# Performance work log

Measured on AMD Instinct MI355X. Metric: run time of the kernel, lower is better.

Reference implementation:

```python
import jax, jax.numpy as jnp
import numpy as np

EPS = 1e-5

def _fftfreq(n, d):
    k = jnp.concatenate([jnp.arange(0, (n + 1) // 2), jnp.arange(-(n // 2), 0)]).astype(jnp.float32)
    return k / (n * d)

def _inorm(x):
    # InstanceNorm2d, no affine, biased variance, eps=1e-5; x: (B,C,H,W)
    m = jnp.mean(x, axis=(-2, -1), keepdims=True)
    v = jnp.var(x, axis=(-2, -1), keepdims=True)
    return (x - m) / jnp.sqrt(v + EPS)

def _spectral_conv(x, t_grid, x_grid, p1, p2, res):
    # x: (B, C, Sx, Sy) real; p1:(in,out,m1) p2:(in,out,m2) res:(in,out,m1,m2) complex64
    B, C, Sx, Sy = x.shape
    dty = x_grid[0, 1] - x_grid[0, 0]
    dtx = t_grid[0, 1] - t_grid[0, 0]
    alpha = jnp.fft.fft2(x, axes=(-2, -1))  # (B,in,Sx,Sy) complex
    om1 = (_fftfreq(Sx, dty) * (2 * jnp.pi) * 1j).astype(jnp.complex64)  # (Sx,)
    om2 = (_fftfreq(Sy, dtx) * (2 * jnp.pi) * 1j).astype(jnp.complex64)  # (Sy,)
    d1 = om1[:, None, None, None] - p1  # (Sx,in,out,m1)
    d2 = om2[:, None, None, None] - p2  # (Sy,in,out,m2)
    denom = jnp.einsum('pbix,qbik->pqbixk', d1, d2)  # (Sx,Sy,in,out,m1,m2)
    Hw = res[None, None] / denom  # pole-residue rational kernel
    r1 = jnp.einsum('biox,oxikpq->bkox', alpha, Hw)  # (B,out,Sx,Sy)
    r2 = jnp.einsum('biox,oxikpq->bkpq', alpha, Hw)  # (B,out,m1,m2)
    x1 = jnp.real(jnp.fft.ifft2(r1, s=(Sx, Sy), axes=(-2, -1)))
    ty_c = x_grid.reshape(1, -1).astype(jnp.complex64)  # (1,Sx)
    tx_c = t_grid.reshape(1, -1).astype(jnp.complex64)  # (1,Sy)
    e1 = jnp.exp(jnp.einsum('bip,kz->bipz', p1, ty_c))  # (in,out,m1,Sx)
    e2 = jnp.exp(jnp.einsum('biq,kx->biqx', p2, tx_c))  # (in,out,m2,Sy)
    term3 = jnp.einsum('bipz,biqx->bipqzx', e1, e2)     # (in,out,m1,m2,Sx,Sy)
    x2 = jnp.real(jnp.einsum('kbpq,bipqzx->kizx', r2, term3)) / (Sx * Sy)
    return x1 + x2

def reference(x, fc0_w, fc0_b, p1r, p1i, p2r, p2i, resr, resi,
              w0_w, w0_b, fc1_w, fc1_b, fc2_w, fc2_b, t_grid, x_grid):
    B, Sx, Sy, _ = x.shape
    gx = jnp.broadcast_to(jnp.linspace(0.0, 1.0, Sx, dtype=jnp.float32)[None, :, None, None], (B, Sx, Sy, 1))
    gy = jnp.broadcast_to(jnp.linspace(0.0, 1.0, Sy, dtype=jnp.float32)[None, None, :, None], (B, Sx, Sy, 1))
    h = jnp.concatenate([x, gx, gy], axis=-1)           # (B,Sx,Sy,3)
    h = h @ fc0_w.T + fc0_b                              # (B,Sx,Sy,16)
    h = h.transpose(0, 3, 1, 2)                          # (B,16,Sx,Sy)
    p1 = (p1r + 1j * p1i).astype(jnp.complex64)
    p2 = (p2r + 1j * p2i).astype(jnp.complex64)
    res = (resr + 1j * resi).astype(jnp.complex64)
    x1 = _inorm(_spectral_conv(_inorm(h), t_grid, x_grid, p1, p2, res))
    x2 = jnp.einsum('bihw,oi->bohw', h, w0_w) + w0_b[None, :, None, None]  # 1x1 conv
    h = x1 + x2
    h = h.transpose(0, 2, 3, 1)                          # (B,Sx,Sy,16)
    h = jnp.sin(h @ fc1_w.T + fc1_b)                     # (B,Sx,Sy,128)
    h = h @ fc2_w.T + fc2_b                              # (B,Sx,Sy,1)
    return h

def setup_inputs() -> dict:
    key = jax.random.key(0)
    ks = jax.random.split(key, 16)
    W, M1, M2, B, S = 16, 4, 5, 4, 64
    scale = 1.0 / (W * W)
    inp = {
        'x': jax.random.normal(ks[0], (B, S, S, 1), jnp.float32),
        'fc0_w': jax.random.normal(ks[1], (W, 3), jnp.float32) * 0.3,
        'fc0_b': jax.random.normal(ks[2], (W,), jnp.float32) * 0.1,
        'p1r': jax.random.uniform(ks[3], (W, W, M1), jnp.float32) * scale,
        'p1i': jax.random.uniform(ks[4], (W, W, M1), jnp.float32) * scale,
        'p2r': jax.random.uniform(ks[5], (W, W, M2), jnp.float32) * scale,
        'p2i': jax.random.uniform(ks[6], (W, W, M2), jnp.float32) * scale,
        'resr': jax.random.uniform(ks[7], (W, W, M1, M2), jnp.float32) * scale,
        'resi': jax.random.uniform(ks[8], (W, W, M1, M2), jnp.float32) * scale,
        'w0_w': jax.random.normal(ks[9], (W, W), jnp.float32) * 0.25,
        'w0_b': jax.random.normal(ks[10], (W,), jnp.float32) * 0.1,
        'fc1_w': jax.random.normal(ks[11], (128, W), jnp.float32) * 0.25,
        'fc1_b': jax.random.normal(ks[12], (128,), jnp.float32) * 0.1,
        'fc2_w': jax.random.normal(ks[13], (1, 128), jnp.float32) * 0.1,
        'fc2_b': jax.random.normal(ks[14], (1,), jnp.float32) * 0.1,
        't_grid': jnp.linspace(0.0, 1.0, S, dtype=jnp.float32).reshape(1, S),
        'x_grid': jnp.linspace(0.0, 1.0, S, dtype=jnp.float32).reshape(1, S),
    }
    return inp
```

## Files before the change

### kernel.cpp

```cpp
#include <hip/hip_runtime.h>

typedef float2 cplx;

constexpr float TWO_PI = 6.28318530717958647692f;

__device__ inline void cmac(float& ax, float& ay, cplx a, cplx b) {
    ax += a.x * b.x - a.y * b.y;
    ay += a.x * b.y + a.y * b.x;
}

__global__ __launch_bounds__(256) void k_pre(
    const float* __restrict__ x, const float* __restrict__ fc0_w,
    const float* __restrict__ fc0_b,
    const float* __restrict__ p1r, const float* __restrict__ p1i,
    const float* __restrict__ p2r, const float* __restrict__ p2i,
    const float* __restrict__ resr, const float* __restrict__ resi,
    const float* __restrict__ t_grid, const float* __restrict__ x_grid,
    cplx* __restrict__ A, cplx* __restrict__ Bq, cplx* __restrict__ Cq,
    cplx* __restrict__ e1, cplx* __restrict__ e2,
    float* __restrict__ h, float* __restrict__ accH2)
{
    int idx = blockIdx.x * 256 + threadIdx.x;
    float dty = x_grid[1] - x_grid[0];
    float dtx = t_grid[1] - t_grid[0];
    const int NA = 65536, NBQ = 81920, NCQ = 81920, NE1 = 65536, NE2 = 81920;
    if (idx < NA) {
        int p = idx & 3, k = (idx >> 2) & 15, i = (idx >> 6) & 15, o = idx >> 10;
        int kf = (o < 32) ? o : o - 64;
        float om = TWO_PI * (float)kf / (64.f * dty);
        float dr = -p1r[(i * 16 + k) * 4 + p], di = om - p1i[(i * 16 + k) * 4 + p];
        float inv = 1.f / (dr * dr + di * di);
        A[idx] = make_float2(dr * inv, -di * inv);
        return;
    }
    idx -= NA;
    if (idx < NBQ) {
        int q = idx % 5, k = (idx / 5) & 15, i = (idx / 80) & 15, xx = idx / 1280;
        int kf = (xx < 32) ? xx : xx - 64;
        float om = TWO_PI * (float)kf / (64.f * dtx);
        float dr = -p2r[(i * 16 + k) * 5 + q], di = om - p2i[(i * 16 + k) * 5 + q];
        float inv = 1.f / (dr * dr + di * di);
        Bq[idx] = make_float2(dr * inv, -di * inv);
        return;
    }
    idx -= NBQ;
    if (idx < NCQ) {
        int q = idx % 5, k = (idx / 5) & 15, i = (idx / 80) & 15, o = idx / 1280;
        int kf = (o < 32) ? o : o - 64;
        float om = TWO_PI * (float)kf / (64.f * dty);
        float cx = 0.f, cy = 0.f;
        for (int p = 0; p < 4; ++p) {
            float dr = -p1r[(i * 16 + k) * 4 + p], di = om - p1i[(i * 16 + k) * 4 + p];
            float inv = 1.f / (dr * dr + di * di);
            float axr = dr * inv, axi = -di * inv;
            float rr = resr[((i * 16 + k) * 4 + p) * 5 + q];
            float ri = resi[((i * 16 + k) * 4 + p) * 5 + q];
            cx += rr * axr - ri * axi;
            cy += rr * axi + ri * axr;
        }
        Cq[idx] = make_float2(cx, cy);
        return;
    }
    idx -= NCQ;
    if (idx < NE1) {
        int z = idx & 63, w = idx >> 6;
        float t = x_grid[z];
        float m = expf(p1r[w] * t);
        float sn, cs; sincosf(p1i[w] * t, &sn, &cs);
        e1[idx] = make_float2(m * cs, m * sn);
        return;
    }
    idx -= NE1;
    if (idx < NE2) {
        int xx = idx & 63, w = idx >> 6;
        float t = t_grid[xx];
        float m = expf(p2r[w] * t);
        float sn, cs; sincosf(p2i[w] * t, &sn, &cs);
        e2[idx] = make_float2(m * cs, m * sn);
        return;
    }
    idx -= NE2;
    {
        int bc = idx >> 12, pix = idx & 4095;
        int b = bc >> 4, c = bc & 15;
        int z = pix >> 6, xx = pix & 63;
        const float inv63 = 1.f / 63.f;
        float v = fc0_w[c * 3] * x[b * 4096 + pix]
                + fc0_w[c * 3 + 1] * (z * inv63)
                + fc0_w[c * 3 + 2] * (xx * inv63) + fc0_b[c];
        h[idx] = v;
        float s = v, s2 = v * v;
        for (int m = 32; m; m >>= 1) {
            s  += __shfl_xor(s,  m, 64);
            s2 += __shfl_xor(s2, m, 64);
        }
        if ((threadIdx.x & 63) == 0) {
            int widx = pix >> 6;
            accH2[bc * 128 + widx * 2]     = s;
            accH2[bc * 128 + widx * 2 + 1] = s2;
        }
    }
}

__global__ __launch_bounds__(256) void k_fftA(
    const float* __restrict__ h, const float* __restrict__ accH2,
    cplx* __restrict__ T1)
{
    __shared__ cplx Ws[64];
    __shared__ float mv[2];
    int bc = blockIdx.x >> 4, pc = blockIdx.x & 15;
    int tid = threadIdx.x;
    if (tid < 64) { float sn, cs; sincosf(-TWO_PI * tid / 64.f, &sn, &cs); Ws[tid] = make_float2(cs, sn); }
    if (tid >= 64 && tid < 128) {
        int l = tid - 64;
        float s  = accH2[bc * 128 + l * 2];
        float s2 = accH2[bc * 128 + l * 2 + 1];
        for (int m = 32; m; m >>= 1) { s += __shfl_xor(s, m, 64); s2 += __shfl_xor(s2, m, 64); }
        if (l == 0) {
            float mean = s * (1.f / 4096.f);
            float var  = s2 * (1.f / 4096.f) - mean * mean;
            mv[0] = mean; mv[1] = rsqrtf(var + 1e-5f);
        }
    }
    __syncthreads();
    float mean = mv[0], rstd = mv[1];
    int j = tid & 63, pl = tid >> 6, p = pc * 4 + pl;
    const float* hb = h + bc * 4096 + j;
    float ax = 0.f, ay = 0.f;
    #pragma unroll 8
    for (int i = 0; i < 64; ++i) {
        float v = hb[i * 64];
        cplx w = Ws[(p * i) & 63];
        ax += v * w.x; ay += v * w.y;
    }
    if (p == 0) ax -= 64.f * mean;
    T1[bc * 4096 + p * 64 + j] = make_float2(ax * rstd, ay * rstd);
}

__global__ __launch_bounds__(256) void k2_fftB(
    const cplx* __restrict__ T1, cplx* __restrict__ alpha, cplx* __restrict__ alphaT)
{
    __shared__ cplx T1s[256];
    int bc = blockIdx.x >> 4, pc = blockIdx.x & 15;
    int tid = threadIdx.x;
    T1s[tid] = T1[bc * 4096 + pc * 256 + tid];
    __syncthreads();
    int q = tid & 63, pl = tid >> 6, p = pc * 4 + pl;
    float c1, s1; sincosf(-TWO_PI * (float)q * (1.f / 64.f), &s1, &c1);
    float wx = 1.f, wy = 0.f;
    float ax = 0.f, ay = 0.f;
    #pragma unroll 8
    for (int j = 0; j < 64; ++j) {
        cplx t = T1s[pl * 64 + j];
        ax += t.x * wx - t.y * wy;
        ay += t.x * wy + t.y * wx;
        float nwx = wx * c1 - wy * s1;
        wy = wx * s1 + wy * c1; wx = nwx;
    }
    cplx v = make_float2(ax, ay);
    alpha [bc * 4096 + p * 64 + q] = v;
    alphaT[(p * 64 + q) * 64 + bc] = v;
}

__global__ __launch_bounds__(64) void k3_r1(
    const cplx* __restrict__ alphaT, const cplx* __restrict__ Cq,
    const cplx* __restrict__ Bq, cplx* __restrict__ r1)
{
    __shared__ cplx Cqs[1280], Bqs[1280], Gs[256], as[64];
    int ox = blockIdx.x; int o = ox >> 6, xx = ox & 63;
    int t = threadIdx.x;
    for (int m = 0; m < 20; ++m) {
        Cqs[m * 64 + t] = Cq[o * 1280 + m * 64 + t];
        Bqs[m * 64 + t] = Bq[xx * 1280 + m * 64 + t];
    }
    as[t] = alphaT[ox * 64 + t];
    __syncthreads();
    for (int m = 0; m < 4; ++m) {
        int e = m * 64 + t; int i = e >> 4, k = e & 15;
        float gx = 0.f, gy = 0.f;
        for (int q = 0; q < 5; ++q) cmac(gx, gy, Cqs[i * 80 + k * 5 + q], Bqs[i * 80 + k * 5 + q]);
        Gs[e] = make_float2(gx, gy);
    }
    __syncthreads();
    int b = t >> 4, k = t & 15;
    float ax = 0.f, ay = 0.f;
    for (int i = 0; i < 16; ++i) cmac(ax, ay, as[b * 16 + i], Gs[i * 16 + k]);
    r1[t * 4096 + ox] = make_float2(ax, ay);
}

__global__ __launch_bounds__(256) void k4_inner1(
    const cplx* __restrict__ alpha, const cplx* __restrict__ Bq,
    cplx* __restrict__ inner1)
{
    int idx = blockIdx.x * 256 + threadIdx.x;
    int kq = idx % 80; int r = idx / 80; int o = r & 63; int bi = r >> 6; int i = bi & 15;
    const cplx* arow = alpha + bi * 4096 + o * 64;
    const cplx* bcol = Bq + i * 80 + kq;
    float ax = 0.f, ay = 0.f;
    #pragma unroll 4
    for (int x = 0; x < 64; ++x) cmac(ax, ay, arow[x], bcol[x * 1280]);
    inner1[idx] = make_float2(ax, ay);
}

__global__ __launch_bounds__(256) void k5_r2(
    const cplx* __restrict__ A, const cplx* __restrict__ inner1,
    const float* __restrict__ resr, const float* __restrict__ resi,
    cplx* __restrict__ r2)
{
    __shared__ cplx red[4][20];
    int bk = blockIdx.x; int b = bk >> 4, k = bk & 15;
    int o = threadIdx.x & 63, ig = threadIdx.x >> 6;
    float accx[4][5] = {}, accy[4][5] = {};
    for (int ii = 0; ii < 4; ++ii) {
        int i = ig * 4 + ii;
        cplx a[4];
        for (int p = 0; p < 4; ++p) a[p] = A[((o * 16 + i) * 16 + k) * 4 + p];
        cplx in[5];
        for (int q = 0; q < 5; ++q) in[q] = inner1[(b * 16 + i) * 5120 + o * 80 + k * 5 + q];
        int rb = (i * 16 + k) * 20;
        for (int p = 0; p < 4; ++p)
            for (int q = 0; q < 5; ++q) {
                float tx = a[p].x * in[q].x - a[p].y * in[q].y;
                float ty = a[p].x * in[q].y + a[p].y * in[q].x;
                float rr = resr[rb + p * 5 + q], ri = resi[rb + p * 5 + q];
                accx[p][q] += rr * tx - ri * ty;
                accy[p][q] += rr * ty + ri * tx;
            }
    }
    for (int m = 32; m; m >>= 1)
        for (int p = 0; p < 4; ++p)
            for (int q = 0; q < 5; ++q) {
                accx[p][q] += __shfl_xor(accx[p][q], m, 64);
                accy[p][q] += __shfl_xor(accy[p][q], m, 64);
            }
    if (o == 0)
        for (int p = 0; p < 4; ++p)
            for (int q = 0; q < 5; ++q)
                red[ig][p * 5 + q] = make_float2(accx[p][q], accy[p][q]);
    __syncthreads();
    if (threadIdx.x < 20) {
        float sx = 0.f, sy = 0.f;
        for (int g = 0; g < 4; ++g) { sx += red[g][threadIdx.x].x; sy += red[g][threadIdx.x].y; }
        r2[bk * 20 + threadIdx.x] = make_float2(sx, sy);
    }
}

__global__ __launch_bounds__(256) void k7_ifftA(
    const cplx* __restrict__ r1, cplx* __restrict__ T2)
{
    __shared__ cplx Ws[64];
    int bk = blockIdx.x >> 4, zc = blockIdx.x & 15;
    int tid = threadIdx.x;
    if (tid < 64) { float sn, cs; sincosf(TWO_PI * tid / 64.f, &sn, &cs); Ws[tid] = make_float2(cs, sn); }
    __syncthreads();
    int j = tid & 63, z = zc * 4 + (tid >> 6);
    const cplx* rr = r1 + bk * 4096 + j;
    float ax = 0.f, ay = 0.f;
    #pragma unroll 4
    for (int o = 0; o < 64; ++o) cmac(ax, ay, rr[o * 64], Ws[(z * o) & 63]);
    T2[bk * 4096 + z * 64 + j] = make_float2(ax, ay);
}

__global__ __launch_bounds__(256) void k8c_sp(
    const cplx* __restrict__ T2, const cplx* __restrict__ r2,
    const cplx* __restrict__ e1, const cplx* __restrict__ e2,
    float* __restrict__ sp, float* __restrict__ accS2)
{
    __shared__ cplx Vs[320];
    __shared__ cplx T2s[256];
    int bc = blockIdx.x >> 4, zc = blockIdx.x & 15;
    int b = bc >> 4, ch = bc & 15;
    int tid = threadIdx.x;
    T2s[tid] = T2[bc * 4096 + zc * 256 + tid];
    for (int e = tid; e < 320; e += 256) {
        int bq = e >> 2, zl = e & 3;
        int bb = bq / 5, q = bq - bb * 5;
        int z = zc * 4 + zl;
        float vx = 0.f, vy = 0.f;
        for (int p = 0; p < 4; ++p)
            cmac(vx, vy, r2[(b * 16 + bb) * 20 + p * 5 + q],
                         e1[((bb * 16 + ch) * 4 + p) * 64 + z]);
        Vs[e] = make_float2(vx, vy);
    }
    __syncthreads();
    int zl = tid >> 6, xx = tid & 63;
    float c1, s1; sincosf(TWO_PI * (float)xx * (1.f / 64.f), &s1, &c1);
    float wx = 1.f, wy = 0.f;
    float acc = 0.f;
    const cplx* trow = &T2s[zl * 64];
    #pragma unroll 8
    for (int j = 0; j < 64; ++j) {
        cplx t = trow[j];
        acc += t.x * wx - t.y * wy;
        float nwx = wx * c1 - wy * s1;
        wy = wx * s1 + wy * c1; wx = nwx;
    }
    const cplx* eb = e2 + ch * 320 + xx;
    #pragma unroll 4
    for (int bb = 0; bb < 16; ++bb)
        for (int q = 0; q < 5; ++q) {
            cplx vv = Vs[(bb * 5 + q) * 4 + zl];
            cplx ee = eb[bb * 5120 + q * 64];
            acc += vv.x * ee.x - vv.y * ee.y;
        }
    float val = acc * (1.f / 4096.f);
    sp[bc * 4096 + zc * 256 + tid] = val;
    float s = val, s2 = val * val;
    for (int m = 32; m; m >>= 1) {
        s  += __shfl_xor(s,  m, 64);
        s2 += __shfl_xor(s2, m, 64);
    }
    if ((tid & 63) == 0) {
        int widx = zc * 4 + (tid >> 6);
        accS2[bc * 128 + widx * 2]     = s;
        accS2[bc * 128 + widx * 2 + 1] = s2;
    }
}

__global__ __launch_bounds__(256) void k9_final(
    const float* __restrict__ sp, const float* __restrict__ accS2,
    const float* __restrict__ h,
    const float* __restrict__ w0_w, const float* __restrict__ w0_b,
    const float* __restrict__ fc1_w, const float* __restrict__ fc1_b,
    const float* __restrict__ fc2_w, const float* __restrict__ fc2_b,
    float* __restrict__ out)
{
    __shared__ float w1s[128 * 16], b1s[128], w2s[128], w0s[256], w0bs[16];
    __shared__ float mvm[16], mvr[16];
    int tid = threadIdx.x;
    int b = blockIdx.x >> 4;
    for (int t = 0; t < 8; ++t) w1s[t * 256 + tid] = fc1_w[t * 256 + tid];
    if (tid < 128) { b1s[tid] = fc1_b[tid]; w2s[tid] = fc2_w[tid]; }
    w0s[tid] = w0_w[tid & 255];
    if (tid < 16) w0bs[tid] = w0_b[tid];
    {
        int wv = tid >> 6, ln = tid & 63;
        for (int cc = 0; cc < 4; ++cc) {
            int c = wv * 4 + cc;
            float s  = accS2[(b * 16 + c) * 128 + ln * 2];
            float s2 = accS2[(b * 16 + c) * 128 + ln * 2 + 1];
            for (int m = 32; m; m >>= 1) { s += __shfl_xor(s, m, 64); s2 += __shfl_xor(s2, m, 64); }
            if (ln == 0) {
                float mean = s * (1.f / 4096.f);
                float var  = s2 * (1.f / 4096.f) - mean * mean;
                mvm[c] = mean; mvr[c] = rsqrtf(var + 1e-5f);
            }
        }
    }
    float b2 = fc2_b[0];
    __syncthreads();
    int pix = blockIdx.x * 256 + tid;
    int rem = pix & 4095;
    float hv[16], tv[16];
    for (int c = 0; c < 16; ++c) {
        hv[c] = h[(b * 16 + c) * 4096 + rem];
        tv[c] = (sp[(b * 16 + c) * 4096 + rem] - mvm[c]) * mvr[c];
    }
    for (int k = 0; k < 16; ++k) {
        float a = w0bs[k];
        for (int c = 0; c < 16; ++c) a += w0s[k * 16 + c] * hv[c];
        tv[k] += a;
    }
    float acc = b2;
    for (int n = 0; n < 128; ++n) {
        float s1 = b1s[n];
        for (int k2 = 0; k2 < 16; ++k2) s1 += w1s[n * 16 + k2] * tv[k2];
        acc += w2s[n] * sinf(s1);
    }
    out[pix] = acc;
}

extern "C" void kernel_launch(void* const* d_in, const int* in_sizes, int n_in,
                              void* d_out, int out_size, void* d_ws, size_t ws_size,
                              hipStream_t stream)
{
    const float* x     = (const float*)d_in[0];
    const float* fc0_w = (const float*)d_in[1];
    const float* fc0_b = (const float*)d_in[2];
    const float* p1r   = (const float*)d_in[3];
    const float* p1i   = (const float*)d_in[4];
    const float* p2r   = (const float*)d_in[5];
    const float* p2i   = (const float*)d_in[6];
    const float* resr  = (const float*)d_in[7];
    const float* resi  = (const float*)d_in[8];
    const float* w0_w  = (const float*)d_in[9];
    const float* w0_b  = (const float*)d_in[10];
    const float* fc1_w = (const float*)d_in[11];
    const float* fc1_b = (const float*)d_in[12];
    const float* fc2_w = (const float*)d_in[13];
    const float* fc2_b = (const float*)d_in[14];
    const float* t_grid= (const float*)d_in[15];
    const float* x_grid= (const float*)d_in[16];
    float* out = (float*)d_out;

    float* ws = (float*)d_ws;
    size_t off = 0;
    float* h      = ws + off; off += 262144;
    cplx*  T1     = (cplx*)(ws + off); off += 524288;
    cplx*  alpha  = (cplx*)(ws + off); off += 524288;
    cplx*  alphaT = (cplx*)(ws + off); off += 524288;
    cplx*  A      = (cplx*)(ws + off); off += 131072;
    cplx*  Bq     = (cplx*)(ws + off); off += 163840;
    cplx*  Cq     = (cplx*)(ws + off); off += 163840;
    cplx*  e1     = (cplx*)(ws + off); off += 131072;
    cplx*  e2     = (cplx*)(ws + off); off += 163840;
    cplx*  r1     = (cplx*)(ws + off); off += 524288;
    cplx*  inner1 = (cplx*)(ws + off); off += 655360;
    cplx*  r2     = (cplx*)(ws + off); off += 2560;
    cplx*  T2     = (cplx*)(ws + off); off += 524288;
    float* sp     = ws + off; off += 262144;
    float* accH2  = ws + off; off += 8192;
    float* accS2  = ws + off; off += 8192;
    (void)ws_size; (void)n_in; (void)in_sizes; (void)out_size;

    k_pre<<<2496, 256, 0, stream>>>(x, fc0_w, fc0_b, p1r, p1i, p2r, p2i, resr, resi,
                                    t_grid, x_grid, A, Bq, Cq, e1, e2, h, accH2);
    k_fftA<<<1024, 256, 0, stream>>>(h, accH2, T1);
    k2_fftB<<<1024, 256, 0, stream>>>(T1, alpha, alphaT);
    k3_r1<<<4096, 64, 0, stream>>>(alphaT, Cq, Bq, r1);
    k4_inner1<<<1280, 256, 0, stream>>>(alpha, Bq, inner1);
    k5_r2<<<64, 256, 0, stream>>>(A, inner1, resr, resi, r2);
    k7_ifftA<<<1024, 256, 0, stream>>>(r1, T2);
    k8c_sp<<<1024, 256, 0, stream>>>(T2, r2, e1, e2, sp, accS2);
    k9_final<<<64, 256, 0, stream>>>(sp, accS2, h, w0_w, w0_b, fc1_w, fc1_b, fc2_w, fc2_b, out);
}
```

Baseline: 202.5 us.

## Fuse FFT stage pairs and r2 contraction into single kernels via shared memory

Merges the two forward DFT passes into one kernel that stages the channel plane in LDS, so the T1 round trip through global memory goes away. The same is done for the inverse DFT and spectral-output kernels, which removes the T2 buffer. The inner1 contraction is folded into the r2 kernel using 1024-thread blocks, and the small reductions are split across two accumulators. Launches and intermediate traffic drop, but each block recomputes full-plane DFTs, LDS use per block rises, and the grids become smaller, with only 64 blocks for r2.

```diff
diff --git a/kernel.cpp b/kernel.cpp
--- a/kernel.cpp
+++ b/kernel.cpp
@@ -102,16 +102,18 @@
     }
 }
 
-__global__ __launch_bounds__(256) void k_fftA(
+__global__ __launch_bounds__(256) void kFFT(
     const float* __restrict__ h, const float* __restrict__ accH2,
-    cplx* __restrict__ T1)
-{
-    __shared__ cplx Ws[64];
+    cplx* __restrict__ alpha, cplx* __restrict__ alphaT)
+{
+    __shared__ float hs[4096];
+    __shared__ cplx  T1s[512];
+    __shared__ cplx  Ws[64];
     __shared__ float mv[2];
-    int bc = blockIdx.x >> 4, pc = blockIdx.x & 15;
+    int bc = blockIdx.x >> 3, pg = blockIdx.x & 7;
     int tid = threadIdx.x;
     if (tid < 64) { float sn, cs; sincosf(-TWO_PI * tid / 64.f, &sn, &cs); Ws[tid] = make_float2(cs, sn); }
-    if (tid >= 64 && tid < 128) {
+    else if (tid < 128) {
         int l = tid - 64;
         float s  = accH2[bc * 128 + l * 2];
         float s2 = accH2[bc * 128 + l * 2 + 1];
@@ -122,44 +124,41 @@
             mv[0] = mean; mv[1] = rsqrtf(var + 1e-5f);
         }
     }
+    for (int t = 0; t < 16; ++t) hs[t * 256 + tid] = h[bc * 4096 + t * 256 + tid];
     __syncthreads();
     float mean = mv[0], rstd = mv[1];
-    int j = tid & 63, pl = tid >> 6, p = pc * 4 + pl;
-    const float* hb = h + bc * 4096 + j;
-    float ax = 0.f, ay = 0.f;
-    #pragma unroll 8
-    for (int i = 0; i < 64; ++i) {
-        float v = hb[i * 64];
-        cplx w = Ws[(p * i) & 63];
-        ax += v * w.x; ay += v * w.y;
-    }
-    if (p == 0) ax -= 64.f * mean;
-    T1[bc * 4096 + p * 64 + j] = make_float2(ax * rstd, ay * rstd);
-}
-
-__global__ __launch_bounds__(256) void k2_fftB(
-    const cplx* __restrict__ T1, cplx* __restrict__ alpha, cplx* __restrict__ alphaT)
-{
-    __shared__ cplx T1s[256];
-    int bc = blockIdx.x >> 4, pc = blockIdx.x & 15;
-    int tid = threadIdx.x;
-    T1s[tid] = T1[bc * 4096 + pc * 256 + tid];
-    __syncthreads();
-    int q = tid & 63, pl = tid >> 6, p = pc * 4 + pl;
-    float c1, s1; sincosf(-TWO_PI * (float)q * (1.f / 64.f), &s1, &c1);
-    float wx = 1.f, wy = 0.f;
-    float ax = 0.f, ay = 0.f;
-    #pragma unroll 8
-    for (int j = 0; j < 64; ++j) {
-        cplx t = T1s[pl * 64 + j];
-        ax += t.x * wx - t.y * wy;
-        ay += t.x * wy + t.y * wx;
-        float nwx = wx * c1 - wy * s1;
-        wy = wx * s1 + wy * c1; wx = nwx;
-    }
-    cplx v = make_float2(ax, ay);
-    alpha [bc * 4096 + p * 64 + q] = v;
-    alphaT[(p * 64 + q) * 64 + bc] = v;
+    for (int t = 0; t < 2; ++t) {
+        int idx = t * 256 + tid;
+        int pl = idx >> 6, j = idx & 63;
+        int p = pg * 8 + pl;
+        float ax0 = 0.f, ay0 = 0.f, ax1 = 0.f, ay1 = 0.f;
+        #pragma unroll
+        for (int i = 0; i < 64; i += 2) {
+            float v0 = hs[i * 64 + j];       cplx w0 = Ws[(p * i) & 63];
+            ax0 += v0 * w0.x; ay0 += v0 * w0.y;
+            float v1 = hs[(i + 1) * 64 + j]; cplx w1 = Ws[(p * (i + 1)) & 63];
+            ax1 += v1 * w1.x; ay1 += v1 * w1.y;
+        }
+        float ax = ax0 + ax1, ay = ay0 + ay1;
+        if (p == 0) ax -= 64.f * mean;
+        T1s[pl * 64 + j] = make_float2(ax * rstd, ay * rstd);
+    }
+    __syncthreads();
+    for (int t = 0; t < 2; ++t) {
+        int idx = t * 256 + tid;
+        int pl = idx >> 6, q = idx & 63;
+        int p = pg * 8 + pl;
+        float ax0 = 0.f, ay0 = 0.f, ax1 = 0.f, ay1 = 0.f;
+        const cplx* trow = &T1s[pl * 64];
+        #pragma unroll
+        for (int j = 0; j < 64; j += 2) {
+            cmac(ax0, ay0, trow[j],     Ws[(q * j) & 63]);
+            cmac(ax1, ay1, trow[j + 1], Ws[(q * (j + 1)) & 63]);
+        }
+        cplx v = make_float2(ax0 + ax1, ay0 + ay1);
+        alpha [bc * 4096 + p * 64 + q] = v;
+        alphaT[(p * 64 + q) * 64 + bc] = v;
+    }
 }
 
 __global__ __launch_bounds__(64) void k3_r1(
@@ -183,49 +182,47 @@
     }
     __syncthreads();
     int b = t >> 4, k = t & 15;
-    float ax = 0.f, ay = 0.f;
-    for (int i = 0; i < 16; ++i) cmac(ax, ay, as[b * 16 + i], Gs[i * 16 + k]);
-    r1[t * 4096 + ox] = make_float2(ax, ay);
-}
-
-__global__ __launch_bounds__(256) void k4_inner1(
+    float ax0 = 0.f, ay0 = 0.f, ax1 = 0.f, ay1 = 0.f;
+    #pragma unroll
+    for (int i = 0; i < 16; i += 2) {
+        cmac(ax0, ay0, as[b * 16 + i],     Gs[i * 16 + k]);
+        cmac(ax1, ay1, as[b * 16 + i + 1], Gs[(i + 1) * 16 + k]);
+    }
+    r1[t * 4096 + ox] = make_float2(ax0 + ax1, ay0 + ay1);
+}
+
+__global__ __launch_bounds__(1024) void k45_r2(
     const cplx* __restrict__ alpha, const cplx* __restrict__ Bq,
-    cplx* __restrict__ inner1)
-{
-    int idx = blockIdx.x * 256 + threadIdx.x;
-    int kq = idx % 80; int r = idx / 80; int o = r & 63; int bi = r >> 6; int i = bi & 15;
-    const cplx* arow = alpha + bi * 4096 + o * 64;
-    const cplx* bcol = Bq + i * 80 + kq;
-    float ax = 0.f, ay = 0.f;
-    #pragma unroll 4
-    for (int x = 0; x < 64; ++x) cmac(ax, ay, arow[x], bcol[x * 1280]);
-    inner1[idx] = make_float2(ax, ay);
-}
-
-__global__ __launch_bounds__(256) void k5_r2(
-    const cplx* __restrict__ A, const cplx* __restrict__ inner1,
+    const cplx* __restrict__ A,
     const float* __restrict__ resr, const float* __restrict__ resi,
     cplx* __restrict__ r2)
 {
-    __shared__ cplx red[4][20];
+    __shared__ cplx red[16][20];
     int bk = blockIdx.x; int b = bk >> 4, k = bk & 15;
-    int o = threadIdx.x & 63, ig = threadIdx.x >> 6;
-    float accx[4][5] = {}, accy[4][5] = {};
-    for (int ii = 0; ii < 4; ++ii) {
-        int i = ig * 4 + ii;
-        cplx a[4];
-        for (int p = 0; p < 4; ++p) a[p] = A[((o * 16 + i) * 16 + k) * 4 + p];
-        cplx in[5];
-        for (int q = 0; q < 5; ++q) in[q] = inner1[(b * 16 + i) * 5120 + o * 80 + k * 5 + q];
-        int rb = (i * 16 + k) * 20;
-        for (int p = 0; p < 4; ++p)
-            for (int q = 0; q < 5; ++q) {
-                float tx = a[p].x * in[q].x - a[p].y * in[q].y;
-                float ty = a[p].x * in[q].y + a[p].y * in[q].x;
-                float rr = resr[rb + p * 5 + q], ri = resi[rb + p * 5 + q];
-                accx[p][q] += rr * tx - ri * ty;
-                accy[p][q] += rr * ty + ri * tx;
-            }
+    int o = threadIdx.x & 63, i = threadIdx.x >> 6;
+    float inx[5] = {}, iny[5] = {};
+    const cplx* arow = alpha + (b * 16 + i) * 4096 + o * 64;
+    const cplx* bq   = Bq + i * 80 + k * 5;
+    #pragma unroll 4
+    for (int xx = 0; xx < 64; ++xx) {
+        cplx av = arow[xx];
+        const cplx* bv = bq + xx * 1280;
+        for (int q = 0; q < 5; ++q) {
+            inx[q] += av.x * bv[q].x - av.y * bv[q].y;
+            iny[q] += av.x * bv[q].y + av.y * bv[q].x;
+        }
+    }
+    float accx[4][5], accy[4][5];
+    int rb = (i * 16 + k) * 20;
+    for (int p = 0; p < 4; ++p) {
+        cplx a = A[((o * 16 + i) * 16 + k) * 4 + p];
+        for (int q = 0; q < 5; ++q) {
+            float tx = a.x * inx[q] - a.y * iny[q];
+            float ty = a.x * iny[q] + a.y * inx[q];
+            float rr = resr[rb + p * 5 + q], ri = resi[rb + p * 5 + q];
+            accx[p][q] = rr * tx - ri * ty;
+            accy[p][q] = rr * ty + ri * tx;
+        }
     }
     for (int m = 32; m; m >>= 1)
         for (int p = 0; p < 4; ++p)
@@ -236,84 +233,87 @@
     if (o == 0)
         for (int p = 0; p < 4; ++p)
             for (int q = 0; q < 5; ++q)
-                red[ig][p * 5 + q] = make_float2(accx[p][q], accy[p][q]);
+                red[i][p * 5 + q] = make_float2(accx[p][q], accy[p][q]);
     __syncthreads();
     if (threadIdx.x < 20) {
         float sx = 0.f, sy = 0.f;
-        for (int g = 0; g < 4; ++g) { sx += red[g][threadIdx.x].x; sy += red[g][threadIdx.x].y; }
+        for (int g = 0; g < 16; ++g) { sx += red[g][threadIdx.x].x; sy += red[g][threadIdx.x].y; }
         r2[bk * 20 + threadIdx.x] = make_float2(sx, sy);
     }
 }
 
-__global__ __launch_bounds__(256) void k7_ifftA(
-    const cplx* __restrict__ r1, cplx* __restrict__ T2)
-{
+__global__ __launch_bounds__(256) void k78_sp(
+    const cplx* __restrict__ r1, const cplx* __restrict__ r2,
+    const cplx* __restrict__ e1, const cplx* __restrict__ e2,
+    float* __restrict__ sp, float* __restrict__ accS2)
+{
+    __shared__ cplx rs[4096];
+    __shared__ cplx T2s[512];
+    __shared__ cplx Vs[640];
     __shared__ cplx Ws[64];
-    int bk = blockIdx.x >> 4, zc = blockIdx.x & 15;
+    int bc = blockIdx.x >> 3, zg = blockIdx.x & 7;
+    int b = bc >> 4, ch = bc & 15;
     int tid = threadIdx.x;
     if (tid < 64) { float sn, cs; sincosf(TWO_PI * tid / 64.f, &sn, &cs); Ws[tid] = make_float2(cs, sn); }
-    __syncthreads();
-    int j = tid & 63, z = zc * 4 + (tid >> 6);
-    const cplx* rr = r1 + bk * 4096 + j;
-    float ax = 0.f, ay = 0.f;
-    #pragma unroll 4
-    for (int o = 0; o < 64; ++o) cmac(ax, ay, rr[o * 64], Ws[(z * o) & 63]);
-    T2[bk * 4096 + z * 64 + j] = make_float2(ax, ay);
-}
-
-__global__ __launch_bounds__(256) void k8c_sp(
-    const cplx* __restrict__ T2, const cplx* __restrict__ r2,
-    const cplx* __restrict__ e1, const cplx* __restrict__ e2,
-    float* __restrict__ sp, float* __restrict__ accS2)
-{
-    __shared__ cplx Vs[320];
-    __shared__ cplx T2s[256];
-    int bc = blockIdx.x >> 4, zc = blockIdx.x & 15;
-    int b = bc >> 4, ch = bc & 15;
-    int tid = threadIdx.x;
-    T2s[tid] = T2[bc * 4096 + zc * 256 + tid];
-    for (int e = tid; e < 320; e += 256) {
-        int bq = e >> 2, zl = e & 3;
+    for (int t = 0; t < 16; ++t) rs[t * 256 + tid] = r1[bc * 4096 + t * 256 + tid];
+    for (int e = tid; e < 640; e += 256) {
+        int zl = e & 7, bq = e >> 3;
         int bb = bq / 5, q = bq - bb * 5;
-        int z = zc * 4 + zl;
+        int z = zg * 8 + zl;
         float vx = 0.f, vy = 0.f;
         for (int p = 0; p < 4; ++p)
             cmac(vx, vy, r2[(b * 16 + bb) * 20 + p * 5 + q],
                          e1[((bb * 16 + ch) * 4 + p) * 64 + z]);
-        Vs[e] = make_float2(vx, vy);
-    }
-    __syncthreads();
-    int zl = tid >> 6, xx = tid & 63;
-    float c1, s1; sincosf(TWO_PI * (float)xx * (1.f / 64.f), &s1, &c1);
-    float wx = 1.f, wy = 0.f;
-    float acc = 0.f;
-    const cplx* trow = &T2s[zl * 64];
-    #pragma unroll 8
-    for (int j = 0; j < 64; ++j) {
-        cplx t = trow[j];
-        acc += t.x * wx - t.y * wy;
-        float nwx = wx * c1 - wy * s1;
-        wy = wx * s1 + wy * c1; wx = nwx;
-    }
-    const cplx* eb = e2 + ch * 320 + xx;
-    #pragma unroll 4
-    for (int bb = 0; bb < 16; ++bb)
-        for (int q = 0; q < 5; ++q) {
-            cplx vv = Vs[(bb * 5 + q) * 4 + zl];
-            cplx ee = eb[bb * 5120 + q * 64];
-            acc += vv.x * ee.x - vv.y * ee.y;
-        }
-    float val = acc * (1.f / 4096.f);
-    sp[bc * 4096 + zc * 256 + tid] = val;
-    float s = val, s2 = val * val;
+        Vs[bq * 8 + zl] = make_float2(vx, vy);
+    }
+    __syncthreads();
+    for (int t = 0; t < 2; ++t) {
+        int idx = t * 256 + tid;
+        int zl = idx >> 6, j = idx & 63;
+        int z = zg * 8 + zl;
+        float ax0 = 0.f, ay0 = 0.f, ax1 = 0.f, ay1 = 0.f;
+        #pragma unroll
+        for (int o = 0; o < 64; o += 2) {
+            cmac(ax0, ay0, rs[o * 64 + j],       Ws[(z * o) & 63]);
+            cmac(ax1, ay1, rs[(o + 1) * 64 + j], Ws[(z * (o + 1)) & 63]);
+        }
+        T2s[zl * 64 + j] = make_float2(ax0 + ax1, ay0 + ay1);
+    }
+    __syncthreads();
+    float s = 0.f, s2 = 0.f;
+    for (int t = 0; t < 2; ++t) {
+        int lp = t * 256 + tid;
+        int zl = lp >> 6, xx = lp & 63;
+        float ax0 = 0.f, ax1 = 0.f;
+        const cplx* trow = &T2s[zl * 64];
+        #pragma unroll
+        for (int j = 0; j < 64; j += 2) {
+            cplx v0 = trow[j];     cplx w0 = Ws[(xx * j) & 63];
+            ax0 += v0.x * w0.x - v0.y * w0.y;
+            cplx v1 = trow[j + 1]; cplx w1 = Ws[(xx * (j + 1)) & 63];
+            ax1 += v1.x * w1.x - v1.y * w1.y;
+        }
+        float acc = ax0 + ax1;
+        const cplx* eb = e2 + ch * 320 + xx;
+        #pragma unroll 4
+        for (int bb = 0; bb < 16; ++bb)
+            for (int q = 0; q < 5; ++q) {
+                cplx vv = Vs[(bb * 5 + q) * 8 + zl];
+                cplx ee = eb[bb * 5120 + q * 64];
+                acc += vv.x * ee.x - vv.y * ee.y;
+            }
+        float val = acc * (1.f / 4096.f);
+        sp[bc * 4096 + zg * 512 + lp] = val;
+        s += val; s2 += val * val;
+    }
     for (int m = 32; m; m >>= 1) {
         s  += __shfl_xor(s,  m, 64);
         s2 += __shfl_xor(s2, m, 64);
     }
     if ((tid & 63) == 0) {
-        int widx = zc * 4 + (tid >> 6);
-        accS2[bc * 128 + widx * 2]     = s;
-        accS2[bc * 128 + widx * 2 + 1] = s2;
+        int widx = zg * 4 + (tid >> 6);
+        accS2[bc * 64 + widx * 2]     = s;
+        accS2[bc * 64 + widx * 2 + 1] = s2;
     }
 }
 
@@ -337,9 +337,12 @@
         int wv = tid >> 6, ln = tid & 63;
         for (int cc = 0; cc < 4; ++cc) {
             int c = wv * 4 + cc;
-            float s  = accS2[(b * 16 + c) * 128 + ln * 2];
-            float s2 = accS2[(b * 16 + c) * 128 + ln * 2 + 1];
-            for (int m = 32; m; m >>= 1) { s += __shfl_xor(s, m, 64); s2 += __shfl_xor(s2, m, 64); }
+            float s = 0.f, s2 = 0.f;
+            if (ln < 32) {
+                s  = accS2[(b * 16 + c) * 64 + ln * 2];
+                s2 = accS2[(b * 16 + c) * 64 + ln * 2 + 1];
+            }
+            for (int m = 16; m; m >>= 1) { s += __shfl_xor(s, m, 64); s2 += __shfl_xor(s2, m, 64); }
             if (ln == 0) {
                 float mean = s * (1.f / 4096.f);
                 float var  = s2 * (1.f / 4096.f) - mean * mean;
@@ -396,7 +399,6 @@
     float* ws = (float*)d_ws;
     size_t off = 0;
     float* h      = ws + off; off += 262144;
-    cplx*  T1     = (cplx*)(ws + off); off += 524288;
     cplx*  alpha  = (cplx*)(ws + off); off += 524288;
     cplx*  alphaT = (cplx*)(ws + off); off += 524288;
     cplx*  A      = (cplx*)(ws + off); off += 131072;
@@ -405,22 +407,17 @@
     cplx*  e1     = (cplx*)(ws + off); off += 131072;
     cplx*  e2     = (cplx*)(ws + off); off += 163840;
     cplx*  r1     = (cplx*)(ws + off); off += 524288;
-    cplx*  inner1 = (cplx*)(ws + off); off += 655360;
     cplx*  r2     = (cplx*)(ws + off); off += 2560;
-    cplx*  T2     = (cplx*)(ws + off); off += 524288;
     float* sp     = ws + off; off += 262144;
     float* accH2  = ws + off; off += 8192;
-    float* accS2  = ws + off; off += 8192;
+    float* accS2  = ws + off; off += 4096;
     (void)ws_size; (void)n_in; (void)in_sizes; (void)out_size;
 
     k_pre<<<2496, 256, 0, stream>>>(x, fc0_w, fc0_b, p1r, p1i, p2r, p2i, resr, resi,
                                     t_grid, x_grid, A, Bq, Cq, e1, e2, h, accH2);
-    k_fftA<<<1024, 256, 0, stream>>>(h, accH2, T1);
-    k2_fftB<<<1024, 256, 0, stream>>>(T1, alpha, alphaT);
+    kFFT<<<512, 256, 0, stream>>>(h, accH2, alpha, alphaT);
     k3_r1<<<4096, 64, 0, stream>>>(alphaT, Cq, Bq, r1);
-    k4_inner1<<<1280, 256, 0, stream>>>(alpha, Bq, inner1);
-    k5_r2<<<64, 256, 0, stream>>>(A, inner1, resr, resi, r2);
-    k7_ifftA<<<1024, 256, 0, stream>>>(r1, T2);
-    k8c_sp<<<1024, 256, 0, stream>>>(T2, r2, e1, e2, sp, accS2);
+    k45_r2<<<64, 1024, 0, stream>>>(alpha, Bq, A, resr, resi, r2);
+    k78_sp<<<512, 256, 0, stream>>>(r1, r2, e1, e2, sp, accS2);
     k9_final<<<64, 256, 0, stream>>>(sp, accS2, h, w0_w, w0_b, fc1_w, fc1_b, fc2_w, fc2_b, out);
 }
```

After: 208.9 us. 1.03x slower.
